# Performance work log

Hardware: AMD Instinct MI355X
Metric: run time of the kernel (lower is better)

Reference implementation:

```python
import jax, jax.numpy as jnp
import numpy as np
from jax import lax

T_DATA = 4096
SUB = 1024
T_HIST = 64
HIST_BASIS = 4
FIX_VAR = 1.0


def setup_inputs() -> dict:
    key = jax.random.key(0)
    ks = jax.random.split(key, 6)
    return {
        "S_conv": jax.random.normal(ks[0], (T_DATA, SUB), dtype=jnp.float32) * 0.5,
        "up_mu_Z": jax.random.normal(ks[1], (T_DATA, SUB), dtype=jnp.float32) * 0.5,
        "noise": jax.random.normal(ks[2], (T_DATA, SUB), dtype=jnp.float32),
        "W_sub": jnp.ones((SUB,), jnp.float32) * 0.25,
        "theta_syn": jax.random.normal(ks[3], (SUB,), dtype=jnp.float32) * 0.1,
        "theta_spike": jnp.ones((SUB,), jnp.float32) * (-1.0),
        "W_spike": jnp.ones((SUB,), jnp.float32) * 1.0,
        "tau_hist": jnp.arange(0.5, 0.5 + HIST_BASIS * 0.5, 0.5, dtype=jnp.float32),
        "K_hist": jax.random.normal(ks[4], (SUB, HIST_BASIS), dtype=jnp.float32) * 0.1,
        "delta_hist": jax.random.uniform(ks[5], (SUB,), dtype=jnp.float32) * 3.0,
    }


def _hist_kernel(tau_hist, K_hist, delta_hist):
    # alpha-function basis kernels: (t/tau) * exp(-t/tau), shifted by delta, clipped at 0
    t = jnp.arange(T_HIST, dtype=jnp.float32)                     # [T_hist]
    tt = jnp.maximum(t[None, :] - delta_hist[:, None], 0.0)      # [sub, T_hist]
    tau = jnp.exp(tau_hist)                                       # [basis]
    ttau = tt[:, :, None] / tau[None, None, :]                    # [sub, T_hist, basis]
    kern = jnp.sum(ttau * jnp.exp(-ttau) * K_hist[:, None, :], axis=-1)  # [sub, T_hist]
    return kern


def _forward(S_conv, up_mu_Z, noise, W_sub, theta_syn, theta_spike, W_spike,
             tau_hist, K_hist, delta_hist):
    kern = _hist_kernel(tau_hist, K_hist, delta_hist)  # kern[s, lag], lag 0 = most recent spike
    # torch flips the kernel then uses conv1d (cross-correlation) over an
    # oldest-first history buffer; equivalent to dotting oldest-first history
    # with the reversed kernel.
    kern_rev = kern[:, ::-1]                           # [sub, T_hist]
    sigma = FIX_VAR ** 0.5

    def step(hist, xs):
        # hist: [sub, T_hist] spike history, oldest first (index T_hist-1 = newest)
        s_t, up_t, n_t = xs
        filtered = jnp.einsum("st,st->s", hist, kern_rev)
        X_in = s_t + filtered + theta_syn
        X_out = jax.nn.sigmoid(X_in)
        Y_t = X_out * W_sub
        down_t = X_out * W_spike + theta_spike
        # (up*prec + down*prec) / (2*prec) == (up + down) / 2
        mu_t = 0.5 * (up_t + down_t)
        Z_out = jax.nn.sigmoid(mu_t + n_t * sigma)
        hist = jnp.concatenate([hist[:, 1:], Z_out[:, None]], axis=1)
        return hist, (Y_t, Z_out, mu_t, down_t)

    hist0 = jnp.zeros((SUB, T_HIST), S_conv.dtype)
    _, (Y, Z, mu_Z, down_mu_Z) = lax.scan(step, hist0, (S_conv, up_mu_Z, noise))
    return Y, Z, mu_Z, down_mu_Z


def reference(S_conv, up_mu_Z, noise, W_sub, theta_syn, theta_spike, W_spike,
              tau_hist, K_hist, delta_hist):
    return _forward(S_conv, up_mu_Z, noise, W_sub, theta_syn, theta_spike,
                    W_spike, tau_hist, K_hist, delta_hist)
```

## Files before the change

kernel.cpp:

```cpp
#include <hip/hip_runtime.h>

#define NL2E (-1.4426950408889634f)

__device__ __forceinline__ float rl(float v, int lane) {
    return __int_as_float(__builtin_amdgcn_readlane(__float_as_int(v), lane));
}
__device__ __forceinline__ float bperm(int byteaddr, float v) {
    return __int_as_float(__builtin_amdgcn_ds_bpermute(byteaddr, __float_as_int(v)));
}

__global__ __launch_bounds__(64) void leaf_integ_kernel(
    const float* __restrict__ S_conv, const float* __restrict__ up_mu_Z,
    const float* __restrict__ noise, const float* __restrict__ W_sub,
    const float* __restrict__ theta_syn, const float* __restrict__ theta_spike,
    const float* __restrict__ W_spike, const float* __restrict__ tau_hist,
    const float* __restrict__ K_hist, const float* __restrict__ delta_hist,
    float* __restrict__ out)
{
    const int SUB = 1024;
    int bid = blockIdx.x;
    int s = ((bid & 7) << 7) + (bid >> 3);
    int l = threadIdx.x;
    bool hi = (l >= 32);
    int pidx = hi ? 1 : 0;
    int rimR = l >> 1;
    int rimC = l & 31;
    int bpaddr = ((((l & 1) ? 32 : 0) + (l >> 1)) << 2);

    __shared__ float lds_rev[128];
    __shared__ float preLds[64];

    float thsyn = theta_syn[s];
    float thspk = theta_spike[s];
    float wsub  = W_sub[s];
    float wspk  = W_spike[s];
    float delta = delta_hist[s];

    float tt = fmaxf((float)l - delta, 0.0f);
    float kern = 0.0f;
    #pragma unroll
    for (int b = 0; b < 4; ++b) {
        float rtau = __expf(-tau_hist[b]);
        float ttau = tt * rtau;
        kern += ttau * __expf(-ttau) * K_hist[s * 4 + b];
    }
    float kvs = NL2E * kern;
    lds_rev[63 - l]  = kvs;
    lds_rev[127 - l] = kvs;
    __syncthreads();

    float k0v = rl(kvs, 0);
    float k1v = rl(kvs, 1);
    float k2v = rl(kvs, 2);
    float kca = hi ? k2v : k1v;
    float kcb = hi ? k1v : k0v;

    const float* krow = &lds_rev[64 - l];

    float thsynS = NL2E * thsyn;
    float c1 = NL2E * 0.5f * wspk;

    float s0raw = S_conv[(size_t)l * SUB + s];
    float s1raw = S_conv[(size_t)(64 + l) * SUB + s];
    float up0   = up_mu_Z[(size_t)l * SUB + s];
    float n0    = noise[(size_t)l * SUB + s];

    float A    = fmaf(s0raw, NL2E, thsynS);
    float sA   = fmaf(s1raw, NL2E, thsynS);
    float preA = NL2E * (fmaf(0.5f, up0, 0.5f * thspk) + n0);
    float upA  = up0;

    float ab01 = hi ? rl(A, 1) : rl(A, 0);
    float xoP  = __builtin_amdgcn_rcpf(1.0f + __builtin_amdgcn_exp2f(ab01));
    float abN  = hi ? rl(A, 3) : rl(A, 2);

    float* Yo = out;
    float* Zo = out + 4194304;
    float* Mo = out + 8388608;
    float* Do = out + 12582912;

    float xcapH = 0.0f, zcapH = 0.0f;
    float pbP = 0.0f;

    for (int B = 0; B < 64; ++B) {
        int t0 = B * 64;
        preLds[l] = preA;
        pbP = hi ? rl(preA, 1) : rl(preA, 0);

        int tP = min(t0 + 128 + l, 4095);
        int tQ = min(t0 + 64 + l, 4095);
        float sB  = S_conv[(size_t)tP * SUB + s];
        float upB = up_mu_Z[(size_t)tQ * SUB + s];
        float nB  = noise[(size_t)tQ * SUB + s];

        #pragma unroll
        for (int i = 0; i < 32; ++i) {
            float klo = krow[2 * i];
            float khi = krow[2 * i + 1];
            float pbN = (i < 31) ? preLds[2 * i + 2 + pidx] : 0.0f;

            float vv = fmaf(xoP, c1, pbP);
            float e2 = __builtin_amdgcn_exp2f(vv);
            float zP = __builtin_amdgcn_rcpf(1.0f + e2);

            bool cap = (rimC == i);
            xcapH = cap ? xoP : xcapH;
            zcapH = cap ? zP  : zcapH;

            float z0 = rl(zP, 0);
            float z1 = rl(zP, 32);

            float Ab = (rimR == i) ? sA : A;
            Ab = fmaf(klo, z0, Ab);
            A  = fmaf(khi, z1, Ab);

            abN = fmaf(kca, z0, abN);
            abN = fmaf(kcb, z1, abN);

            float e1 = __builtin_amdgcn_exp2f(abN);
            xoP = __builtin_amdgcn_rcpf(1.0f + e1);

            float alo = rl(A, (2 * i + 4) & 63);
            float ahi = rl(A, (2 * i + 5) & 63);
            abN = hi ? ahi : alo;

            pbP = pbN;
        }

        float xcap = bperm(bpaddr, xcapH);
        float zcap = bperm(bpaddr, zcapH);

        float down = fmaf(xcap, wspk, thspk);
        float Yv   = xcap * wsub;
        float mu   = 0.5f * (upA + down);
        size_t o = (size_t)(t0 + l) * SUB + s;
        Yo[o] = Yv; Zo[o] = zcap; Mo[o] = mu; Do[o] = down;

        sA   = fmaf(sB, NL2E, thsynS);
        preA = NL2E * (fmaf(0.5f, upB, 0.5f * thspk) + nB);
        upA  = upB;
    }
}

extern "C" void kernel_launch(void* const* d_in, const int* in_sizes, int n_in,
                              void* d_out, int out_size, void* d_ws, size_t ws_size,
                              hipStream_t stream) {
    const float* S_conv     = (const float*)d_in[0];
    const float* up_mu_Z    = (const float*)d_in[1];
    const float* noise      = (const float*)d_in[2];
    const float* W_sub      = (const float*)d_in[3];
    const float* theta_syn  = (const float*)d_in[4];
    const float* theta_spike= (const float*)d_in[5];
    const float* W_spike    = (const float*)d_in[6];
    const float* tau_hist   = (const float*)d_in[7];
    const float* K_hist     = (const float*)d_in[8];
    const float* delta_hist = (const float*)d_in[9];
    float* out = (float*)d_out;

    leaf_integ_kernel<<<dim3(1024), dim3(64), 0, stream>>>(
        S_conv, up_mu_Z, noise, W_sub, theta_syn, theta_spike, W_spike,
        tau_hist, K_hist, delta_hist, out);
}
```

Baseline: 130.4 us.

## Deepen recurrence lookahead to two steps to shorten the serial dependency chain

The scan's per-step critical path is restructured so the next X_out is computed from a near accumulator right after z is broadcast, while a second far accumulator is advanced for the step after. The readlane of the accumulated history sum now happens two steps ahead instead of one, and the LDS kernel-coefficient and pre-activation loads are software-pipelined across iterations. The aim is to take the readlane and FMA latency off the serial exp/rcp chain. It adds registers and extra FMAs per step, and correctness depends on the lane-offset bookkeeping across block boundaries.

New measurement: 232.9 us. 78.6% more time.

```diff
diff --git a/kernel.cpp b/kernel.cpp
--- a/kernel.cpp
+++ b/kernel.cpp
@@ -49,11 +49,11 @@
     lds_rev[127 - l] = kvs;
     __syncthreads();
 
-    float k0v = rl(kvs, 0);
-    float k1v = rl(kvs, 1);
-    float k2v = rl(kvs, 2);
-    float kca = hi ? k2v : k1v;
-    float kcb = hi ? k1v : k0v;
+    float k1v = rl(kvs, 1), k2v = rl(kvs, 2), k3v = rl(kvs, 3), k4v = rl(kvs, 4);
+    float kNa = hi ? k2v : k1v;
+    float kNb = hi ? k1v : 0.0f;
+    float kFa = hi ? k4v : k3v;
+    float kFb = hi ? k3v : k2v;
 
     const float* krow = &lds_rev[64 - l];
 
@@ -70,23 +70,25 @@
     float preA = NL2E * (fmaf(0.5f, up0, 0.5f * thspk) + n0);
     float upA  = up0;
 
-    float ab01 = hi ? rl(A, 1) : rl(A, 0);
-    float xoP  = __builtin_amdgcn_rcpf(1.0f + __builtin_amdgcn_exp2f(ab01));
-    float abN  = hi ? rl(A, 3) : rl(A, 2);
+    preLds[l] = preA;
+
+    float ab0 = hi ? rl(A, 1) : rl(A, 0);
+    float xoP = __builtin_amdgcn_rcpf(1.0f + __builtin_amdgcn_exp2f(ab0));
+    float ab1 = hi ? rl(A, 3) : rl(A, 2);
+    float ab2 = hi ? rl(A, 5) : rl(A, 4);
+    float pbP = hi ? rl(preA, 1) : rl(preA, 0);
+    float klo = krow[0];
+    float khi = krow[1];
+
+    float xcapH = 0.0f, zcapH = 0.0f;
 
     float* Yo = out;
     float* Zo = out + 4194304;
     float* Mo = out + 8388608;
     float* Do = out + 12582912;
 
-    float xcapH = 0.0f, zcapH = 0.0f;
-    float pbP = 0.0f;
-
     for (int B = 0; B < 64; ++B) {
         int t0 = B * 64;
-        preLds[l] = preA;
-        pbP = hi ? rl(preA, 1) : rl(preA, 0);
-
         int tP = min(t0 + 128 + l, 4095);
         int tQ = min(t0 + 64 + l, 4095);
         float sB  = S_conv[(size_t)tP * SUB + s];
@@ -95,41 +97,34 @@
 
         #pragma unroll
         for (int i = 0; i < 32; ++i) {
-            float klo = krow[2 * i];
-            float khi = krow[2 * i + 1];
-            float pbN = (i < 31) ? preLds[2 * i + 2 + pidx] : 0.0f;
-
             float vv = fmaf(xoP, c1, pbP);
             float e2 = __builtin_amdgcn_exp2f(vv);
             float zP = __builtin_amdgcn_rcpf(1.0f + e2);
-
+            float z0 = rl(zP, 0);
+            float z1 = rl(zP, 32);
+            ab1 = fmaf(kNa, z0, ab1);
+            ab1 = fmaf(kNb, z1, ab1);
+            float e1 = __builtin_amdgcn_exp2f(ab1);
+            float xoN = __builtin_amdgcn_rcpf(1.0f + e1);
+            ab2 = fmaf(kFa, z0, ab2);
+            ab2 = fmaf(kFb, z1, ab2);
             bool cap = (rimC == i);
             xcapH = cap ? xoP : xcapH;
             zcapH = cap ? zP  : zcapH;
-
-            float z0 = rl(zP, 0);
-            float z1 = rl(zP, 32);
-
             float Ab = (rimR == i) ? sA : A;
             Ab = fmaf(klo, z0, Ab);
             A  = fmaf(khi, z1, Ab);
-
-            abN = fmaf(kca, z0, abN);
-            abN = fmaf(kcb, z1, abN);
-
-            float e1 = __builtin_amdgcn_exp2f(abN);
-            xoP = __builtin_amdgcn_rcpf(1.0f + e1);
-
-            float alo = rl(A, (2 * i + 4) & 63);
-            float ahi = rl(A, (2 * i + 5) & 63);
-            abN = hi ? ahi : alo;
-
-            pbP = pbN;
+            int jl = (2 * i + 2) & 63;
+            float kloN = krow[jl];
+            float khiN = krow[jl + 1];
+            int p0 = (2 * i + 6) & 63, p1 = (2 * i + 7) & 63;
+            float a3 = hi ? rl(A, p1) : rl(A, p0);
+            float pbN = (i < 31) ? preLds[2 * i + 2 + pidx] : 0.0f;
+            xoP = xoN; ab1 = ab2; ab2 = a3; pbP = pbN; klo = kloN; khi = khiN;
         }
 
         float xcap = bperm(bpaddr, xcapH);
         float zcap = bperm(bpaddr, zcapH);
-
         float down = fmaf(xcap, wspk, thspk);
         float Yv   = xcap * wsub;
         float mu   = 0.5f * (upA + down);
@@ -139,6 +134,8 @@
         sA   = fmaf(sB, NL2E, thsynS);
         preA = NL2E * (fmaf(0.5f, upB, 0.5f * thspk) + nB);
         upA  = upB;
+        preLds[l] = preA;
+        pbP = hi ? rl(preA, 1) : rl(preA, 0);
     }
 }
 
```
